# Kernel optimization log

Hardware: AMD Instinct MI355X
Metric: run time of the kernel (lower is better)

## Reference

```python
import jax, jax.numpy as jnp
import numpy as np

D_MODEL, D_KV, N_HEADS = 1024, 64, 16
NUM_BUCKETS, MAX_DIST = 32, 128
B, S = 2, 2048


def _relative_position_bucket(relative_position, num_buckets=NUM_BUCKETS, max_distance=MAX_DIST):
    # bidirectional=True branch of the TF code
    nb = num_buckets // 2
    n = -relative_position
    ret = (n < 0).astype(jnp.int32) * nb
    n = jnp.abs(n)
    max_exact = nb // 2
    is_small = n < max_exact
    val_if_large = max_exact + (
        jnp.log(n.astype(jnp.float32) / max_exact)
        / np.log(max_distance / max_exact)
        * (nb - max_exact)
    ).astype(jnp.int32)
    val_if_large = jnp.minimum(val_if_large, nb - 1)
    return ret + jnp.where(is_small, n, val_if_large)


def compute_bias(rel_emb, qlen, klen):
    ctx = jnp.arange(qlen)[:, None]
    mem = jnp.arange(klen)[None, :]
    rp_bucket = _relative_position_bucket(mem - ctx)  # [q, k]
    values = rel_emb[rp_bucket]                       # [q, k, h]
    return jnp.transpose(values, (2, 0, 1))[None]     # [1, h, q, k]


def setup_inputs() -> dict:
    key = jax.random.key(0)
    ks = jax.random.split(key, 6)
    sc = 1.0 / np.sqrt(D_MODEL)
    return {
        "inputs": jax.random.normal(ks[0], (B, S, D_MODEL), jnp.float32),
        "Wq": jax.random.normal(ks[1], (D_MODEL, N_HEADS * D_KV), jnp.float32) * sc,
        "Wk": jax.random.normal(ks[2], (D_MODEL, N_HEADS * D_KV), jnp.float32) * sc,
        "Wv": jax.random.normal(ks[3], (D_MODEL, N_HEADS * D_KV), jnp.float32) * sc,
        "Wo": jax.random.normal(ks[4], (N_HEADS * D_KV, D_MODEL), jnp.float32) * sc,
        "rel_emb": jax.random.normal(ks[5], (NUM_BUCKETS, N_HEADS), jnp.float32),
    }


def reference(inputs, Wq, Wk, Wv, Wo, rel_emb):
    bs, qlen, _ = inputs.shape

    def split_heads(x):
        return jnp.transpose(x.reshape(bs, -1, N_HEADS, D_KV), (0, 2, 1, 3))

    q = split_heads(inputs @ Wq)  # [b, h, s, d]
    k = split_heads(inputs @ Wk)
    v = split_heads(inputs @ Wv)

    position_bias = compute_bias(rel_emb, qlen, qlen)      # [1, h, q, k]
    scores = jnp.einsum('bnqd,bnkd->bnqk', q, k) + position_bias  # NOTE: no 1/sqrt(d) scaling (T5 style)
    attn = jax.nn.softmax(scores, axis=-1)
    hidden = jnp.einsum('bnqk,bnkd->bnqd', attn, v)
    hidden = jnp.transpose(hidden, (0, 2, 1, 3)).reshape(bs, qlen, N_HEADS * D_KV)
    return hidden @ Wo
```

## Files before the change

### kernel.cpp

```cpp
#include <hip/hip_runtime.h>


typedef __attribute__((ext_vector_type(8))) short s16x8;
typedef __attribute__((ext_vector_type(4))) float f32x4;
typedef __attribute__((ext_vector_type(16))) float f32x16;
typedef __attribute__((ext_vector_type(2))) unsigned int u32x2;

__device__ __forceinline__ unsigned short f2bf(float f) {
  unsigned int u = __float_as_uint(f);
  u = (u + 0x7fffu + ((u >> 16) & 1u)) >> 16;
  return (unsigned short)u;
}

__device__ __forceinline__ unsigned cvtpk(float lo, float hi) {
  unsigned r;
  asm("v_cvt_pk_bf16_f32 %0, %1, %2" : "=v"(r) : "v"(lo), "v"(hi));
  return r;
}

#define GLD16(g, l)                                              \
  __builtin_amdgcn_global_load_lds(                              \
      (const __attribute__((address_space(1))) void*)(g),        \
      (__attribute__((address_space(3))) void*)(l), 16, 0, 0)

__global__ __launch_bounds__(256) void cvt_lin(const float* __restrict__ in,
                                               unsigned short* __restrict__ out,
                                               int n4) {
  int i = blockIdx.x * 256 + threadIdx.x;
  int stride = gridDim.x * 256;
  for (; i < n4; i += stride) {
    float4 v = ((const float4*)in)[i];
    ushort4 o;
    o.x = f2bf(v.x); o.y = f2bf(v.y); o.z = f2bf(v.z); o.w = f2bf(v.w);
    ((ushort4*)out)[i] = o;
  }
}

__global__ __launch_bounds__(256) void cvt_trans4(const float* __restrict__ W0,
                                                  const float* __restrict__ W1,
                                                  const float* __restrict__ W2,
                                                  const float* __restrict__ W3,
                                                  unsigned short* __restrict__ Dqkv,
                                                  unsigned short* __restrict__ Do_) {
  const int z = blockIdx.z;
  const float* W = (z == 0) ? W0 : (z == 1) ? W1 : (z == 2) ? W2 : W3;
  unsigned short* WT = (z < 3) ? (Dqkv + (size_t)z * 1024 * 1024) : Do_;
  __shared__ float t[32][33];
  int n0 = blockIdx.x * 32, k0 = blockIdx.y * 32;
  int tx = threadIdx.x & 31, ty = threadIdx.x >> 5;
#pragma unroll
  for (int i = 0; i < 32; i += 8)
    t[ty + i][tx] = W[(size_t)(k0 + ty + i) * 1024 + n0 + tx];
  __syncthreads();
#pragma unroll
  for (int i = 0; i < 32; i += 8)
    WT[(size_t)(n0 + ty + i) * 1024 + k0 + tx] = f2bf(t[tx][ty + i]);
}

__global__ __launch_bounds__(256) void bias_tab_k(const float* __restrict__ rel,
                                                  float* __restrict__ tab) {
  int idx = blockIdx.x * 256 + threadIdx.x;
  int h = idx >> 12, di = idx & 4095;
  int delta = di - 2047;
  int n = -delta;
  int ret = (n < 0) ? 16 : 0;
  n = n < 0 ? -n : n;
  int bucket;
  if (n < 8) {
    bucket = ret + n;
  } else {
    float lf = (float)log((double)n * 0.125);
    float f = lf / 2.772588722239781f * 8.0f;
    int v = 8 + (int)f;
    bucket = ret + (v < 15 ? v : 15);
  }
  tab[idx] = rel[bucket * 16 + h] * 1.4426950408889634f;
}

__global__ __launch_bounds__(256, 2) void gemm_qkv(
    const unsigned short* __restrict__ A, const unsigned short* __restrict__ BT,
    unsigned short* __restrict__ O0, unsigned short* __restrict__ O1,
    unsigned short* __restrict__ O2) {
  __shared__ __align__(16) unsigned short aT[128 * 64];
  __shared__ __align__(16) unsigned short bT[128 * 64];
  const int tid = threadIdx.x;
  const int lane = tid & 63, w = tid >> 6;
  const int l15 = lane & 15, l4 = lane >> 4;
  const int m0 = blockIdx.y * 128, n0 = blockIdx.x * 128;
  const int wr = w >> 1, wc = w & 1;

  const f32x4 fzero = {0.f, 0.f, 0.f, 0.f};
  f32x4 acc[4][4];
#pragma unroll
  for (int i = 0; i < 4; ++i)
#pragma unroll
    for (int j = 0; j < 4; ++j) acc[i][j] = fzero;

  for (int k0 = 0; k0 < 1024; k0 += 64) {
#pragma unroll
    for (int p = 0; p < 4; ++p) {
      int slot = (p * 4 + w) * 64 + lane;
      int row = slot >> 3, s = slot & 7;
      int ks = (s ^ (row & 7)) << 3;
      GLD16(A + (size_t)(m0 + row) * 1024 + k0 + ks, (char*)aT + (p * 4 + w) * 1024);
      GLD16(BT + (size_t)(n0 + row) * 1024 + k0 + ks, (char*)bT + (p * 4 + w) * 1024);
    }
    __syncthreads();
#pragma unroll
    for (int kk = 0; kk < 2; ++kk) {
      int slotk = kk * 4 + l4;
      s16x8 af[4], bfr[4];
#pragma unroll
      for (int mi = 0; mi < 4; ++mi) {
        int row = wr * 64 + mi * 16 + l15;
        af[mi] = *(const s16x8*)(aT + row * 64 + ((slotk ^ (row & 7)) << 3));
      }
#pragma unroll
      for (int nj = 0; nj < 4; ++nj) {
        int row = wc * 64 + nj * 16 + l15;
        bfr[nj] = *(const s16x8*)(bT + row * 64 + ((slotk ^ (row & 7)) << 3));
      }
      __builtin_amdgcn_s_setprio(1);
#pragma unroll
      for (int mi = 0; mi < 4; ++mi)
#pragma unroll
        for (int nj = 0; nj < 4; ++nj)
          acc[mi][nj] = __builtin_amdgcn_mfma_f32_16x16x32_bf16(af[mi], bfr[nj], acc[mi][nj], 0, 0, 0);
      __builtin_amdgcn_s_setprio(0);
    }
    __syncthreads();
  }

#pragma unroll
  for (int mi = 0; mi < 4; ++mi)
#pragma unroll
    for (int nj = 0; nj < 4; ++nj)
#pragma unroll
      for (int r = 0; r < 4; ++r) {
        int row = m0 + wr * 64 + mi * 16 + l4 * 4 + r;
        int col = n0 + wc * 64 + nj * 16 + l15;
        int which = col >> 10;
        int cc = col & 1023;
        int b = row >> 11, s2 = row & 2047, hh = cc >> 6, d = cc & 63;
        if (which == 0)
          O0[((size_t)((b * 16 + hh) * 2048 + s2)) * 64 + d] =
              f2bf(acc[mi][nj][r] * 1.4426950408889634f);
        else if (which == 1)
          O1[((size_t)((b * 16 + hh) * 2048 + s2)) * 64 + d] = f2bf(acc[mi][nj][r]);
        else
          O2[((size_t)((b * 16 + hh) * 64 + d)) * 2048 + s2] = f2bf(acc[mi][nj][r]);
      }
}

__global__ __launch_bounds__(256, 2) void gemm_op(
    const unsigned short* __restrict__ A, const unsigned short* __restrict__ BT,
    float* __restrict__ O) {
  __shared__ __align__(16) unsigned short aT[128 * 64];
  __shared__ __align__(16) unsigned short bT[64 * 64];
  const int tid = threadIdx.x;
  const int lane = tid & 63, w = tid >> 6;
  const int l15 = lane & 15, l4 = lane >> 4;
  const int m0 = blockIdx.y * 128, n0 = blockIdx.x * 64;
  const int wr = w >> 1, wc = w & 1;

  const f32x4 fzero = {0.f, 0.f, 0.f, 0.f};
  f32x4 acc[4][2];
#pragma unroll
  for (int i = 0; i < 4; ++i)
#pragma unroll
    for (int j = 0; j < 2; ++j) acc[i][j] = fzero;

  for (int k0 = 0; k0 < 1024; k0 += 64) {
#pragma unroll
    for (int p = 0; p < 4; ++p) {
      int slot = (p * 4 + w) * 64 + lane;
      int row = slot >> 3, s = slot & 7;
      int ks = (s ^ (row & 7)) << 3;
      GLD16(A + (size_t)(m0 + row) * 1024 + k0 + ks, (char*)aT + (p * 4 + w) * 1024);
    }
#pragma unroll
    for (int p = 0; p < 2; ++p) {
      int slot = (p * 4 + w) * 64 + lane;
      int row = slot >> 3, s = slot & 7;
      int ks = (s ^ (row & 7)) << 3;
      GLD16(BT + (size_t)(n0 + row) * 1024 + k0 + ks, (char*)bT + (p * 4 + w) * 1024);
    }
    __syncthreads();
#pragma unroll
    for (int kk = 0; kk < 2; ++kk) {
      int slotk = kk * 4 + l4;
      s16x8 af[4], bfr[2];
#pragma unroll
      for (int mi = 0; mi < 4; ++mi) {
        int row = wr * 64 + mi * 16 + l15;
        af[mi] = *(const s16x8*)(aT + row * 64 + ((slotk ^ (row & 7)) << 3));
      }
#pragma unroll
      for (int nj = 0; nj < 2; ++nj) {
        int row = wc * 32 + nj * 16 + l15;
        bfr[nj] = *(const s16x8*)(bT + row * 64 + ((slotk ^ (row & 7)) << 3));
      }
      __builtin_amdgcn_s_setprio(1);
#pragma unroll
      for (int mi = 0; mi < 4; ++mi)
#pragma unroll
        for (int nj = 0; nj < 2; ++nj)
          acc[mi][nj] = __builtin_amdgcn_mfma_f32_16x16x32_bf16(af[mi], bfr[nj], acc[mi][nj], 0, 0, 0);
      __builtin_amdgcn_s_setprio(0);
    }
    __syncthreads();
  }

#pragma unroll
  for (int mi = 0; mi < 4; ++mi)
#pragma unroll
    for (int nj = 0; nj < 2; ++nj)
#pragma unroll
      for (int r = 0; r < 4; ++r) {
        int row = m0 + wr * 64 + mi * 16 + l4 * 4 + r;
        int col = n0 + wc * 32 + nj * 16 + l15;
        O[(size_t)row * 1024 + col] = acc[mi][nj][r];
      }
}

__global__ __launch_bounds__(256, 2) void attn_k(
    const unsigned short* __restrict__ Q,
    const unsigned short* __restrict__ K,
    const unsigned short* __restrict__ VT,
    const float* __restrict__ btab,
    unsigned short* __restrict__ H) {
  __shared__ __align__(16) unsigned short k_lds[3][64 * 64];
  __shared__ __align__(16) unsigned short v_lds[3][64 * 64];
  const int tid = threadIdx.x;
  const int lane = tid & 63, w = tid >> 6;
  const int l31 = lane & 31, l5 = lane >> 5;
  const int bh = blockIdx.y, h = bh & 15, b = bh >> 4;
  const int q0 = blockIdx.x * 128 + w * 32;
  const unsigned short* Qp = Q + (size_t)bh * 2048 * 64;
  const unsigned short* Kp = K + (size_t)bh * 2048 * 64;
  const unsigned short* Vp = VT + (size_t)bh * 64 * 2048;
  const float* btq = btab + h * 4096 + 2047 - (q0 + l31) + 4 * l5;

#define STAGE(buf, kvv)                                                              \
  {                                                                                  \
    _Pragma("unroll") for (int p_ = 0; p_ < 2; ++p_) {                               \
      int slot_ = (p_ * 4 + w) * 64 + lane;                                          \
      int row_ = slot_ >> 3, s_ = slot_ & 7;                                         \
      int ks_ = (s_ ^ (row_ & 7)) << 3;                                              \
      GLD16(Kp + (size_t)((kvv) + row_) * 64 + ks_,                                  \
            (char*)k_lds[buf] + (p_ * 4 + w) * 1024);                                \
      GLD16(Vp + (size_t)row_ * 2048 + (kvv) + ks_,                                  \
            (char*)v_lds[buf] + (p_ * 4 + w) * 1024);                                \
    }                                                                                \
  }

#define LOADB(dst, kvv)                                                              \
  {                                                                                  \
    _Pragma("unroll") for (int t_ = 0; t_ < 2; ++t_)                                 \
      _Pragma("unroll") for (int r_ = 0; r_ < 16; ++r_)                              \
        dst[t_ * 16 + r_] = btq[(kvv) + t_ * 32 + (r_ & 3) + 8 * (r_ >> 2)];         \
  }

  s16x8 qf[4];
#pragma unroll
  for (int ks = 0; ks < 4; ++ks)
    qf[ks] = *(const s16x8*)(Qp + (size_t)(q0 + l31) * 64 + ks * 16 + l5 * 8);

  f32x16 oacc[2];
#pragma unroll
  for (int r = 0; r < 16; ++r) { oacc[0][r] = 0.f; oacc[1][r] = 0.f; }
  float s4[4] = {0.f, 0.f, 0.f, 0.f};

  float ba[32], bb[32];
  LOADB(ba, 0);
  STAGE(0, 0);
  STAGE(1, 64);
  __syncthreads();
  int ib = 0;

#define BODY(IB, KVV, BC, BN_)                                                       \
  {                                                                                  \
    const int kvv = (KVV);                                                           \
    int nb_ = (IB) + 2; if (nb_ >= 3) nb_ -= 3;                                      \
    if (kvv + 128 < 2048) STAGE(nb_, kvv + 128);                                     \
    f32x16 st[2];                                                                    \
    _Pragma("unroll") for (int t = 0; t < 2; ++t)                                    \
      _Pragma("unroll") for (int r = 0; r < 16; ++r)                                 \
        st[t][r] = BC[t * 16 + r];                                                   \
    if (kvv + 64 < 2048) LOADB(BN_, kvv + 64);                                       \
    const char* kl = (const char*)k_lds[IB];                                         \
    __builtin_amdgcn_s_setprio(1);                                                   \
    _Pragma("unroll") for (int ks = 0; ks < 4; ++ks) {                               \
      int sl = ks * 2 + l5;                                                          \
      int sw = (sl ^ (l31 & 7)) << 4;                                                \
      s16x8 ka0 = *(const s16x8*)(kl + l31 * 128 + sw);                              \
      s16x8 ka1 = *(const s16x8*)(kl + (32 + l31) * 128 + sw);                       \
      st[0] = __builtin_amdgcn_mfma_f32_32x32x16_bf16(ka0, qf[ks], st[0], 0, 0, 0);  \
      st[1] = __builtin_amdgcn_mfma_f32_32x32x16_bf16(ka1, qf[ks], st[1], 0, 0, 0);  \
    }                                                                                \
    __builtin_amdgcn_s_setprio(0);                                                   \
             \
    _Pragma("unroll") for (int t = 0; t < 2; ++t)                                    \
      _Pragma("unroll") for (int r = 0; r < 16; ++r) {                               \
        float p_ = exp2f(st[t][r]);                                                  \
        st[t][r] = p_;                                                               \
        s4[r & 3] += p_;                                                             \
      }                                                                              \
    s16x8 pb[4];                                                                     \
    _Pragma("unroll") for (int t = 0; t < 2; ++t)                                    \
      _Pragma("unroll") for (int hh = 0; hh < 2; ++hh) {                             \
        unsigned cA = cvtpk(st[t][hh * 8 + 0], st[t][hh * 8 + 1]);                   \
        unsigned cB = cvtpk(st[t][hh * 8 + 2], st[t][hh * 8 + 3]);                   \
        unsigned cC = cvtpk(st[t][hh * 8 + 4], st[t][hh * 8 + 5]);                   \
        unsigned cD = cvtpk(st[t][hh * 8 + 6], st[t][hh * 8 + 7]);                   \
        u32x2 s1 = __builtin_amdgcn_permlane32_swap(cA, cC, false, false);           \
        u32x2 s2 = __builtin_amdgcn_permlane32_swap(cB, cD, false, false);           \
        union { unsigned u[4]; s16x8 v; } pu;                                        \
        pu.u[0] = s1.x; pu.u[1] = s2.x; pu.u[2] = s1.y; pu.u[3] = s2.y;              \
        pb[t * 2 + hh] = pu.v;                                                       \
      }                                                                              \
    const char* vl = (const char*)v_lds[IB];                                         \
    __builtin_amdgcn_s_setprio(1);                                                   \
    _Pragma("unroll") for (int ks2 = 0; ks2 < 4; ++ks2) {                            \
      int sl = ks2 * 2 + l5;                                                         \
      int sw = (sl ^ (l31 & 7)) << 4;                                                \
      s16x8 va0 = *(const s16x8*)(vl + l31 * 128 + sw);                              \
      s16x8 va1 = *(const s16x8*)(vl + (32 + l31) * 128 + sw);                       \
      oacc[0] = __builtin_amdgcn_mfma_f32_32x32x16_bf16(va0, pb[ks2], oacc[0], 0, 0, 0); \
      oacc[1] = __builtin_amdgcn_mfma_f32_32x32x16_bf16(va1, pb[ks2], oacc[1], 0, 0, 0); \
    }                                                                                \
    __builtin_amdgcn_s_setprio(0);                                                   \
    __syncthreads();                                                                 \
  }

  for (int s = 0; s < 16; ++s) {
    BODY(ib, s * 128, ba, bb);
    ib = (ib == 2) ? 0 : ib + 1;
    BODY(ib, s * 128 + 64, bb, ba);
    ib = (ib == 2) ? 0 : ib + 1;
  }
#undef BODY
#undef LOADB
#undef STAGE

  float sum = (s4[0] + s4[1]) + (s4[2] + s4[3]);
  u32x2 rs = __builtin_amdgcn_permlane32_swap(__float_as_uint(sum), __float_as_uint(sum), false, false);
  float lrun = __uint_as_float(rs.x) + __uint_as_float(rs.y);

  float inv = 1.0f / lrun;
  size_t hb = (((size_t)(b * 2048 + q0 + l31)) * 1024 + h * 64 + 4 * l5) * 2;
#pragma unroll
  for (int nd = 0; nd < 2; ++nd)
#pragma unroll
    for (int g = 0; g < 4; ++g) {
      unsigned w0 = cvtpk(oacc[nd][g * 4 + 0] * inv, oacc[nd][g * 4 + 1] * inv);
      unsigned w1 = cvtpk(oacc[nd][g * 4 + 2] * inv, oacc[nd][g * 4 + 3] * inv);
      unsigned long long pk8 = (unsigned long long)w0 | ((unsigned long long)w1 << 32);
      *(unsigned long long*)((char*)H + hb + (nd * 32 + 8 * g) * 2) = pk8;
    }
}

extern "C" void kernel_launch(void* const* d_in, const int* in_sizes, int n_in,
                              void* d_out, int out_size, void* d_ws, size_t ws_size,
                              hipStream_t stream) {
  const float* X   = (const float*)d_in[0];
  const float* Wq  = (const float*)d_in[1];
  const float* Wk  = (const float*)d_in[2];
  const float* Wv  = (const float*)d_in[3];
  const float* Wo  = (const float*)d_in[4];
  const float* rel = (const float*)d_in[5];

  char* ws = (char*)d_ws;
  unsigned short* Xb     = (unsigned short*)(ws);
  unsigned short* Hid    = Xb;
  unsigned short* WqkvT  = (unsigned short*)(ws + (8u << 20));
  unsigned short* WoT    = (unsigned short*)(ws + (14u << 20));
  unsigned short* Qb     = (unsigned short*)(ws + (16u << 20));
  unsigned short* Kb     = (unsigned short*)(ws + (24u << 20));
  unsigned short* VTb    = (unsigned short*)(ws + (32u << 20));
  float* btab            = (float*)(ws + (40u << 20));

  cvt_lin<<<1024, 256, 0, stream>>>(X, Xb, (2 * 2048 * 1024) / 4);
  cvt_trans4<<<dim3(32, 32, 4), 256, 0, stream>>>(Wq, Wk, Wv, Wo, WqkvT, WoT);
  bias_tab_k<<<256, 256, 0, stream>>>(rel, btab);

  gemm_qkv<<<dim3(24, 32), 256, 0, stream>>>(Xb, WqkvT, Qb, Kb, VTb);

  attn_k<<<dim3(16, 32), 256, 0, stream>>>(Qb, Kb, VTb, btab, Hid);

  gemm_op<<<dim3(16, 32), 256, 0, stream>>>(Hid, WoT, (float*)d_out);
}
```

Measured before the change: 139.8 us.

## Split KV range across two wave groups in attention and merge partials via LDS

The attention kernel now runs 512 threads per block. Each group of four waves processes half of the key/value sequence with double-buffered LDS staging, and the partial outputs and row sums are reduced through shared memory before normalization. This raises in-flight waves per CU and shortens each wave's serial KV loop. The cost is a final LDS reduction and tighter register limits from the launch bounds. Separately, the bias-table kernel is merged into the weight-conversion launch as an extra grid slice, and exp2 uses the hardware builtin when available.

Measured after the change: 228.0 us. +63.1%, slower.

```diff
diff --git a/kernel.cpp b/kernel.cpp
--- a/kernel.cpp
+++ b/kernel.cpp
@@ -5,6 +5,12 @@
 typedef __attribute__((ext_vector_type(4))) float f32x4;
 typedef __attribute__((ext_vector_type(16))) float f32x16;
 typedef __attribute__((ext_vector_type(2))) unsigned int u32x2;
+
+#if __has_builtin(__builtin_amdgcn_exp2f)
+#define EXP2(x) __builtin_amdgcn_exp2f(x)
+#else
+#define EXP2(x) exp2f(x)
+#endif
 
 __device__ __forceinline__ unsigned short f2bf(float f) {
   unsigned int u = __float_as_uint(f);
@@ -36,13 +42,35 @@
   }
 }
 
-__global__ __launch_bounds__(256) void cvt_trans4(const float* __restrict__ W0,
-                                                  const float* __restrict__ W1,
-                                                  const float* __restrict__ W2,
-                                                  const float* __restrict__ W3,
-                                                  unsigned short* __restrict__ Dqkv,
-                                                  unsigned short* __restrict__ Do_) {
+__global__ __launch_bounds__(256) void cvt_prep(const float* __restrict__ W0,
+                                                const float* __restrict__ W1,
+                                                const float* __restrict__ W2,
+                                                const float* __restrict__ W3,
+                                                const float* __restrict__ rel,
+                                                unsigned short* __restrict__ Dqkv,
+                                                unsigned short* __restrict__ Do_,
+                                                float* __restrict__ tab) {
   const int z = blockIdx.z;
+  if (z == 4) {
+    int idx = (blockIdx.y * 32 + blockIdx.x) * 256 + threadIdx.x;
+    if (idx >= 16 * 4096) return;
+    int h = idx >> 12, di = idx & 4095;
+    int delta = di - 2047;
+    int n = -delta;
+    int ret = (n < 0) ? 16 : 0;
+    n = n < 0 ? -n : n;
+    int bucket;
+    if (n < 8) {
+      bucket = ret + n;
+    } else {
+      float lf = (float)log((double)n * 0.125);
+      float f = lf / 2.772588722239781f * 8.0f;
+      int v = 8 + (int)f;
+      bucket = ret + (v < 15 ? v : 15);
+    }
+    tab[idx] = rel[bucket * 16 + h] * 1.4426950408889634f;
+    return;
+  }
   const float* W = (z == 0) ? W0 : (z == 1) ? W1 : (z == 2) ? W2 : W3;
   unsigned short* WT = (z < 3) ? (Dqkv + (size_t)z * 1024 * 1024) : Do_;
   __shared__ float t[32][33];
@@ -55,26 +83,6 @@
 #pragma unroll
   for (int i = 0; i < 32; i += 8)
     WT[(size_t)(n0 + ty + i) * 1024 + k0 + tx] = f2bf(t[tx][ty + i]);
-}
-
-__global__ __launch_bounds__(256) void bias_tab_k(const float* __restrict__ rel,
-                                                  float* __restrict__ tab) {
-  int idx = blockIdx.x * 256 + threadIdx.x;
-  int h = idx >> 12, di = idx & 4095;
-  int delta = di - 2047;
-  int n = -delta;
-  int ret = (n < 0) ? 16 : 0;
-  n = n < 0 ? -n : n;
-  int bucket;
-  if (n < 8) {
-    bucket = ret + n;
-  } else {
-    float lf = (float)log((double)n * 0.125);
-    float f = lf / 2.772588722239781f * 8.0f;
-    int v = 8 + (int)f;
-    bucket = ret + (v < 15 ? v : 15);
-  }
-  tab[idx] = rel[bucket * 16 + h] * 1.4426950408889634f;
 }
 
 __global__ __launch_bounds__(256, 2) void gemm_qkv(
@@ -223,35 +231,35 @@
       }
 }
 
-__global__ __launch_bounds__(256, 2) void attn_k(
+__global__ __launch_bounds__(512, 4) void attn_k(
     const unsigned short* __restrict__ Q,
     const unsigned short* __restrict__ K,
     const unsigned short* __restrict__ VT,
     const float* __restrict__ btab,
     unsigned short* __restrict__ H) {
-  __shared__ __align__(16) unsigned short k_lds[3][64 * 64];
-  __shared__ __align__(16) unsigned short v_lds[3][64 * 64];
+  __shared__ __align__(16) char smem[65536];
   const int tid = threadIdx.x;
   const int lane = tid & 63, w = tid >> 6;
   const int l31 = lane & 31, l5 = lane >> 5;
+  const int half = w >> 2;
+  const int q0 = blockIdx.x * 128 + (w & 3) * 32;
   const int bh = blockIdx.y, h = bh & 15, b = bh >> 4;
-  const int q0 = blockIdx.x * 128 + w * 32;
   const unsigned short* Qp = Q + (size_t)bh * 2048 * 64;
   const unsigned short* Kp = K + (size_t)bh * 2048 * 64;
   const unsigned short* Vp = VT + (size_t)bh * 64 * 2048;
-  const float* btq = btab + h * 4096 + 2047 - (q0 + l31) + 4 * l5;
+  const float* btq = btab + h * 4096 + 2047 - (q0 + l31) + 4 * l5 + half * 1024;
 
 #define STAGE(buf, kvv)                                                              \
   {                                                                                  \
-    _Pragma("unroll") for (int p_ = 0; p_ < 2; ++p_) {                               \
-      int slot_ = (p_ * 4 + w) * 64 + lane;                                          \
-      int row_ = slot_ >> 3, s_ = slot_ & 7;                                         \
-      int ks_ = (s_ ^ (row_ & 7)) << 3;                                              \
-      GLD16(Kp + (size_t)((kvv) + row_) * 64 + ks_,                                  \
-            (char*)k_lds[buf] + (p_ * 4 + w) * 1024);                                \
-      GLD16(Vp + (size_t)row_ * 2048 + (kvv) + ks_,                                  \
-            (char*)v_lds[buf] + (p_ * 4 + w) * 1024);                                \
-    }                                                                                \
+    int row_ = tid >> 3, s_ = tid & 7;                                               \
+    int ks_ = (s_ ^ (row_ & 7)) << 3;                                                \
+    GLD16(Kp + (size_t)((kvv) + row_) * 64 + ks_, smem + (buf) * 8192 + tid * 16);   \
+    GLD16(Kp + (size_t)(1024 + (kvv) + row_) * 64 + ks_,                             \
+          smem + 32768 + (buf) * 8192 + tid * 16);                                   \
+    GLD16(Vp + (size_t)row_ * 2048 + (kvv) + ks_,                                    \
+          smem + 16384 + (buf) * 8192 + tid * 16);                                   \
+    GLD16(Vp + (size_t)row_ * 2048 + 1024 + (kvv) + ks_,                             \
+          smem + 16384 + 32768 + (buf) * 8192 + tid * 16);                           \
   }
 
 #define LOADB(dst, kvv)                                                              \
@@ -274,21 +282,21 @@
   float ba[32], bb[32];
   LOADB(ba, 0);
   STAGE(0, 0);
-  STAGE(1, 64);
   __syncthreads();
-  int ib = 0;
-
-#define BODY(IB, KVV, BC, BN_)                                                       \
+  int cur = 0;
+  const char* kbase = smem + half * 32768;
+  const char* vbase = smem + half * 32768 + 16384;
+
+#define BODY(KVV, BC, BN_)                                                           \
   {                                                                                  \
     const int kvv = (KVV);                                                           \
-    int nb_ = (IB) + 2; if (nb_ >= 3) nb_ -= 3;                                      \
-    if (kvv + 128 < 2048) STAGE(nb_, kvv + 128);                                     \
+    if (kvv + 64 < 1024) STAGE(cur ^ 1, kvv + 64);                                   \
     f32x16 st[2];                                                                    \
     _Pragma("unroll") for (int t = 0; t < 2; ++t)                                    \
       _Pragma("unroll") for (int r = 0; r < 16; ++r)                                 \
         st[t][r] = BC[t * 16 + r];                                                   \
-    if (kvv + 64 < 2048) LOADB(BN_, kvv + 64);                                       \
-    const char* kl = (const char*)k_lds[IB];                                         \
+    if (kvv + 64 < 1024) LOADB(BN_, kvv + 64);                                       \
+    const char* kl = kbase + cur * 8192;                                             \
     __builtin_amdgcn_s_setprio(1);                                                   \
     _Pragma("unroll") for (int ks = 0; ks < 4; ++ks) {                               \
       int sl = ks * 2 + l5;                                                          \
@@ -299,10 +307,9 @@
       st[1] = __builtin_amdgcn_mfma_f32_32x32x16_bf16(ka1, qf[ks], st[1], 0, 0, 0);  \
     }                                                                                \
     __builtin_amdgcn_s_setprio(0);                                                   \
-             \
     _Pragma("unroll") for (int t = 0; t < 2; ++t)                                    \
       _Pragma("unroll") for (int r = 0; r < 16; ++r) {                               \
-        float p_ = exp2f(st[t][r]);                                                  \
+        float p_ = EXP2(st[t][r]);                                                   \
         st[t][r] = p_;                                                               \
         s4[r & 3] += p_;                                                             \
       }                                                                              \
@@ -319,7 +326,7 @@
         pu.u[0] = s1.x; pu.u[1] = s2.x; pu.u[2] = s1.y; pu.u[3] = s2.y;              \
         pb[t * 2 + hh] = pu.v;                                                       \
       }                                                                              \
-    const char* vl = (const char*)v_lds[IB];                                         \
+    const char* vl = vbase + cur * 8192;                                             \
     __builtin_amdgcn_s_setprio(1);                                                   \
     _Pragma("unroll") for (int ks2 = 0; ks2 < 4; ++ks2) {                            \
       int sl = ks2 * 2 + l5;                                                         \
@@ -331,13 +338,12 @@
     }                                                                                \
     __builtin_amdgcn_s_setprio(0);                                                   \
     __syncthreads();                                                                 \
-  }
-
-  for (int s = 0; s < 16; ++s) {
-    BODY(ib, s * 128, ba, bb);
-    ib = (ib == 2) ? 0 : ib + 1;
-    BODY(ib, s * 128 + 64, bb, ba);
-    ib = (ib == 2) ? 0 : ib + 1;
+    cur ^= 1;                                                                        \
+  }
+
+  for (int s = 0; s < 8; ++s) {
+    BODY(s * 128, ba, bb);
+    BODY(s * 128 + 64, bb, ba);
   }
 #undef BODY
 #undef LOADB
@@ -345,19 +351,32 @@
 
   float sum = (s4[0] + s4[1]) + (s4[2] + s4[3]);
   u32x2 rs = __builtin_amdgcn_permlane32_swap(__float_as_uint(sum), __float_as_uint(sum), false, false);
-  float lrun = __uint_as_float(rs.x) + __uint_as_float(rs.y);
-
-  float inv = 1.0f / lrun;
-  size_t hb = (((size_t)(b * 2048 + q0 + l31)) * 1024 + h * 64 + 4 * l5) * 2;
-#pragma unroll
-  for (int nd = 0; nd < 2; ++nd)
-#pragma unroll
-    for (int g = 0; g < 4; ++g) {
-      unsigned w0 = cvtpk(oacc[nd][g * 4 + 0] * inv, oacc[nd][g * 4 + 1] * inv);
-      unsigned w1 = cvtpk(oacc[nd][g * 4 + 2] * inv, oacc[nd][g * 4 + 3] * inv);
-      unsigned long long pk8 = (unsigned long long)w0 | ((unsigned long long)w1 << 32);
-      *(unsigned long long*)((char*)H + hb + (nd * 32 + 8 * g) * 2) = pk8;
-    }
+  float lsum = __uint_as_float(rs.x) + __uint_as_float(rs.y);
+
+  float* comb = (float*)smem;
+  if (w >= 4) {
+    float* p = comb + ((w - 4) * 64 + lane) * 34;
+#pragma unroll
+    for (int r = 0; r < 16; ++r) { p[r] = oacc[0][r]; p[16 + r] = oacc[1][r]; }
+    p[32] = lsum;
+  }
+  __syncthreads();
+  if (w < 4) {
+    const float* p = comb + (w * 64 + lane) * 34;
+#pragma unroll
+    for (int r = 0; r < 16; ++r) { oacc[0][r] += p[r]; oacc[1][r] += p[16 + r]; }
+    float inv = 1.0f / (lsum + p[32]);
+    size_t hb = (((size_t)(b * 2048 + q0 + l31)) * 1024 + h * 64 + 4 * l5) * 2;
+#pragma unroll
+    for (int nd = 0; nd < 2; ++nd)
+#pragma unroll
+      for (int g = 0; g < 4; ++g) {
+        unsigned w0 = cvtpk(oacc[nd][g * 4 + 0] * inv, oacc[nd][g * 4 + 1] * inv);
+        unsigned w1 = cvtpk(oacc[nd][g * 4 + 2] * inv, oacc[nd][g * 4 + 3] * inv);
+        unsigned long long pk8 = (unsigned long long)w0 | ((unsigned long long)w1 << 32);
+        *(unsigned long long*)((char*)H + hb + (nd * 32 + 8 * g) * 2) = pk8;
+      }
+  }
 }
 
 extern "C" void kernel_launch(void* const* d_in, const int* in_sizes, int n_in,
@@ -381,12 +400,11 @@
   float* btab            = (float*)(ws + (40u << 20));
 
   cvt_lin<<<1024, 256, 0, stream>>>(X, Xb, (2 * 2048 * 1024) / 4);
-  cvt_trans4<<<dim3(32, 32, 4), 256, 0, stream>>>(Wq, Wk, Wv, Wo, WqkvT, WoT);
-  bias_tab_k<<<256, 256, 0, stream>>>(rel, btab);
+  cvt_prep<<<dim3(32, 32, 5), 256, 0, stream>>>(Wq, Wk, Wv, Wo, rel, WqkvT, WoT, btab);
 
   gemm_qkv<<<dim3(24, 32), 256, 0, stream>>>(Xb, WqkvT, Qb, Kb, VTb);
 
-  attn_k<<<dim3(16, 32), 256, 0, stream>>>(Qb, Kb, VTb, btab, Hid);
+  attn_k<<<dim3(16, 32), 512, 0, stream>>>(Qb, Kb, VTb, btab, Hid);
 
   gemm_op<<<dim3(16, 32), 256, 0, stream>>>(Hid, WoT, (float*)d_out);
 }
```
